# Optimization experiments

Hardware: AMD Instinct MI355X
Metric: run time of the kernel (lower is better)

The kernel has to match this reference:

```python
import jax, jax.numpy as jnp
import numpy as np

LAMBDA_DECAY = 0.01   # self.lambda_decay
ALPHA = 0.95          # self.alpha_continuity
TAU = 0.0             # self.tau
LN_EPS = 1e-5

M, D = 8192, 4096


def layer_norm(x):
    m = jnp.mean(x, axis=-1, keepdims=True)
    v = jnp.var(x, axis=-1, keepdims=True)
    return (x - m) / jnp.sqrt(v + LN_EPS)


def setup_inputs() -> dict:
    key = jax.random.key(0)
    k1, k2, k3, k4, k5 = jax.random.split(key, 5)
    return {
        "states": jax.random.normal(k1, (M, D), dtype=jnp.float32),       # memory bank cell states
        "weights": jax.random.uniform(k2, (M,), dtype=jnp.float32),        # per-cell weights
        "timestamps": jax.random.uniform(k3, (M,), dtype=jnp.float32),     # per-cell timestamps
        "current_state": jax.random.normal(k4, (D,), dtype=jnp.float32),
        "sensed_state": jax.random.normal(k5, (D,), dtype=jnp.float32),    # appended to bank; not in output math
        "t_new": jnp.ones((1,), dtype=jnp.float32),
    }


def reference(states, weights, timestamps, current_state, sensed_state, t_new):
    # Batched per-cell decay update (replaces the Python loop with .item() syncs):
    # cell.weight *= exp(-lambda * |(t_new - cell.timestamp) - tau|)
    decay = jnp.exp(-LAMBDA_DECAY * jnp.abs((t_new[0] - timestamps) - TAU))  # [M]
    w = weights * decay                                                       # [M]

    # scaled_dot single-query attention over the memory bank, modulated by cell weights
    scale = 1.0 / jnp.sqrt(jnp.asarray(states.shape[-1], dtype=states.dtype))
    scores = (states @ current_state) * scale        # [M]
    attn = jax.nn.softmax(scores)                    # [M]
    wa = attn * w
    wa = wa / (jnp.sum(wa) + 1e-9)                   # renormalize by decayed cell weights
    attention_out = wa @ states                      # [D]

    # recursive update: new = alpha * current + (1 - alpha) * attention_out
    new_state = ALPHA * current_state + (1.0 - ALPHA) * attention_out

    # layer norm of the new persistent state
    return layer_norm(new_state)
```

## Files before the change

kernel.cpp:

```cpp
#include <hip/hip_runtime.h>
#include <math.h>

#define LAMBDA_DECAY 0.01f
#define ALPHA 0.95f
#define LN_EPS 1e-5f

#define NB 512
#define RPB 16
#define WPB 8
#define K2Y 32

typedef float v4f __attribute__((ext_vector_type(4)));

static __device__ __forceinline__ float wave_sum_all(float v) {
#pragma unroll
    for (int o = 32; o > 0; o >>= 1) v += __shfl_xor(v, o);
    return v;
}

static __device__ float block_sum(float v, float* sh, int nwaves) {
    int lane = threadIdx.x & 63;
    int w = threadIdx.x >> 6;
    v = wave_sum_all(v);
    if (lane == 0) sh[w] = v;
    __syncthreads();
    float r = 0.0f;
    for (int i = 0; i < nwaves; ++i) r += sh[i];
    __syncthreads();
    return r;
}

__global__ __launch_bounds__(512) void fused_kernel(
    const float* __restrict__ states, const float* __restrict__ cur,
    const float* __restrict__ weights, const float* __restrict__ ts,
    const float* __restrict__ t_new,
    float* __restrict__ partial, float* __restrict__ partE, float* __restrict__ partS,
    int M, int D, float scale)
{
    __shared__ float shp[2][WPB];

    const int wid = threadIdx.x >> 6;
    const int lane = threadIdx.x & 63;
    const int r0 = blockIdx.x * RPB;
    const int f4base = wid * 128 + lane;
    const int rstride = D >> 2;

    const float tn = t_new[0];

    const v4f* c4 = (const v4f*)cur;
    const v4f curp0 = c4[f4base];
    const v4f curp1 = c4[f4base + 64];

    v4f acc0 = (v4f)(0.0f), acc1 = (v4f)(0.0f);
    float E = 0.0f, S = 0.0f;

    const v4f* sp = (const v4f*)states;

    v4f rv[2][2];
    rv[0][0] = sp[(size_t)r0 * rstride + f4base];
    rv[0][1] = sp[(size_t)r0 * rstride + f4base + 64];

#pragma unroll
    for (int r = 0; r < RPB; ++r) {
        const int row = r0 + r;
        const int cb = r & 1;
        const int nb = cb ^ 1;

        if (r + 1 < RPB) {
            rv[nb][0] = sp[(size_t)(row + 1) * rstride + f4base];
            rv[nb][1] = sp[(size_t)(row + 1) * rstride + f4base + 64];
        }

        const v4f a0 = rv[cb][0], a1 = rv[cb][1];

        float d0 = 0.0f, d1 = 0.0f;
        d0 = fmaf(a0[0], curp0[0], d0); d1 = fmaf(a1[0], curp1[0], d1);
        d0 = fmaf(a0[1], curp0[1], d0); d1 = fmaf(a1[1], curp1[1], d1);
        d0 = fmaf(a0[2], curp0[2], d0); d1 = fmaf(a1[2], curp1[2], d1);
        d0 = fmaf(a0[3], curp0[3], d0); d1 = fmaf(a1[3], curp1[3], d1);
        float pd = wave_sum_all(d0 + d1);

        if (lane == 0) shp[cb][wid] = pd;
        __syncthreads();

        float s = 0.0f;
#pragma unroll
        for (int w = 0; w < WPB; ++w) s += shp[cb][w];
        s *= scale;

        const float e = expf(s);
        const float wgt = weights[row] * expf(-LAMBDA_DECAY * fabsf(tn - ts[row]));
        const float p = e * wgt;
        E += e; S += p;

        acc0 += p * a0;
        acc1 += p * a1;
    }

    v4f* pb = (v4f*)(partial + (size_t)blockIdx.x * D);
    pb[f4base] = acc0;
    pb[f4base + 64] = acc1;
    if (threadIdx.x == 0) {
        partE[blockIdx.x] = E;
        partS[blockIdx.x] = S;
    }
}

__global__ __launch_bounds__(256) void reduce_kernel(
    const float* __restrict__ partial, float* __restrict__ attn_raw, int D)
{
    const int col = blockIdx.x * 256 + threadIdx.x;
    const int b0 = blockIdx.y * (NB / K2Y);
    float a0 = 0.0f, a1 = 0.0f, a2 = 0.0f, a3 = 0.0f;
#pragma unroll
    for (int b = 0; b < NB / K2Y; b += 4) {
        a0 += partial[(size_t)(b0 + b) * D + col];
        a1 += partial[(size_t)(b0 + b + 1) * D + col];
        a2 += partial[(size_t)(b0 + b + 2) * D + col];
        a3 += partial[(size_t)(b0 + b + 3) * D + col];
    }
    atomicAdd(&attn_raw[col], (a0 + a1) + (a2 + a3));
}

__global__ __launch_bounds__(1024) void finalize_kernel(
    const float* __restrict__ attn_raw, const float* __restrict__ partE,
    const float* __restrict__ partS, const float* __restrict__ cur,
    float* __restrict__ out, int D)
{
    __shared__ float sh[16];
    const int tid = threadIdx.x;

    float E = 0.0f, S = 0.0f;
    for (int i = tid; i < NB; i += 1024) { E += partE[i]; S += partS[i]; }
    E = block_sum(E, sh, 16);
    S = block_sum(S, sh, 16);
    const float inv = 1.0f / (S + 1e-9f * E);

    float v[4];
    float s = 0.0f, s2 = 0.0f;
#pragma unroll
    for (int k = 0; k < 4; ++k) {
        const int c = tid + k * 1024;
        const float nv = ALPHA * cur[c] + (1.0f - ALPHA) * (attn_raw[c] * inv);
        v[k] = nv;
        s += nv; s2 += nv * nv;
    }
    s = block_sum(s, sh, 16);
    s2 = block_sum(s2, sh, 16);
    const float mean = s / (float)D;
    const float var = s2 / (float)D - mean * mean;
    const float rstd = 1.0f / sqrtf(var + LN_EPS);
#pragma unroll
    for (int k = 0; k < 4; ++k)
        out[tid + k * 1024] = (v[k] - mean) * rstd;
}

extern "C" void kernel_launch(void* const* d_in, const int* in_sizes, int n_in,
                              void* d_out, int out_size, void* d_ws, size_t ws_size,
                              hipStream_t stream) {
    const float* states     = (const float*)d_in[0];
    const float* weights    = (const float*)d_in[1];
    const float* timestamps = (const float*)d_in[2];
    const float* current    = (const float*)d_in[3];
    const float* t_new      = (const float*)d_in[5];
    float* out = (float*)d_out;

    const int M = in_sizes[1];
    const int D = in_sizes[3];

    float* ws       = (float*)d_ws;
    float* partial  = ws;
    float* partE    = partial + (size_t)NB * D;
    float* partS    = partE + NB;
    float* attn_raw = partS + NB;

    const float scale = 1.0f / sqrtf((float)D);

    hipMemsetAsync(attn_raw, 0, (size_t)D * sizeof(float), stream);

    fused_kernel<<<NB, 512, 0, stream>>>(
        states, current, weights, timestamps, t_new,
        partial, partE, partS, M, D, scale);

    {
        dim3 grid(D / 256, K2Y);
        reduce_kernel<<<grid, 256, 0, stream>>>(partial, attn_raw, D);
    }

    finalize_kernel<<<1, 1024, 0, stream>>>(attn_raw, partE, partS, current, out, D);
}
```

Baseline: 39.61 us.

## Fuse reduce and finalize into one tail kernel with last-block counter

Removes the memset by having block 0 of the main kernel zero the accumulator and counter, and merges the column-reduce and layernorm-finalize kernels into one tail kernel. The tail kernel uses a global atomic counter so the last finishing block performs the normalization and layer norm. This cuts two launches and their gaps, but the reduction now runs on only 32 blocks, each summing 256 partial rows per column, which lowers parallelism for reading the 8 MB partial buffer.

Measured after the change: 44.62 us. +12.7%, slower.

```diff
diff --git a/kernel.cpp b/kernel.cpp
--- a/kernel.cpp
+++ b/kernel.cpp
@@ -8,7 +8,7 @@
 #define NB 512
 #define RPB 16
 #define WPB 8
-#define K2Y 32
+#define TB 32
 
 typedef float v4f __attribute__((ext_vector_type(4)));
 
@@ -35,6 +35,7 @@
     const float* __restrict__ weights, const float* __restrict__ ts,
     const float* __restrict__ t_new,
     float* __restrict__ partial, float* __restrict__ partE, float* __restrict__ partS,
+    float* __restrict__ attn_raw, unsigned* __restrict__ counter,
     int M, int D, float scale)
 {
     __shared__ float shp[2][WPB];
@@ -44,6 +45,11 @@
     const int r0 = blockIdx.x * RPB;
     const int f4base = wid * 128 + lane;
     const int rstride = D >> 2;
+
+    if (blockIdx.x == 0) {
+        for (int d = threadIdx.x; d < D; d += 512) attn_raw[d] = 0.0f;
+        if (threadIdx.x == 0) *counter = 0u;
+    }
 
     const float tn = t_new[0];
 
@@ -106,53 +112,67 @@
     }
 }
 
-__global__ __launch_bounds__(256) void reduce_kernel(
-    const float* __restrict__ partial, float* __restrict__ attn_raw, int D)
-{
-    const int col = blockIdx.x * 256 + threadIdx.x;
-    const int b0 = blockIdx.y * (NB / K2Y);
-    float a0 = 0.0f, a1 = 0.0f, a2 = 0.0f, a3 = 0.0f;
-#pragma unroll
-    for (int b = 0; b < NB / K2Y; b += 4) {
-        a0 += partial[(size_t)(b0 + b) * D + col];
-        a1 += partial[(size_t)(b0 + b + 1) * D + col];
-        a2 += partial[(size_t)(b0 + b + 2) * D + col];
-        a3 += partial[(size_t)(b0 + b + 3) * D + col];
-    }
-    atomicAdd(&attn_raw[col], (a0 + a1) + (a2 + a3));
-}
-
-__global__ __launch_bounds__(1024) void finalize_kernel(
-    const float* __restrict__ attn_raw, const float* __restrict__ partE,
+__global__ __launch_bounds__(256) void tail_kernel(
+    const float* __restrict__ partial, const float* __restrict__ partE,
     const float* __restrict__ partS, const float* __restrict__ cur,
+    float* __restrict__ attn_raw, unsigned* __restrict__ counter,
     float* __restrict__ out, int D)
 {
-    __shared__ float sh[16];
-    const int tid = threadIdx.x;
+    __shared__ float shc[128];
+    __shared__ float sh16[16];
+    __shared__ unsigned sdone;
+
+    const int cid = threadIdx.x & 127;
+    const int half = threadIdx.x >> 7;
+    const int col = blockIdx.x * 128 + cid;
+
+    {
+        const int b0 = half * (NB / 2);
+        float a0 = 0.0f, a1 = 0.0f, a2 = 0.0f, a3 = 0.0f;
+        for (int b = 0; b < NB / 2; b += 4) {
+            a0 += partial[(size_t)(b0 + b) * D + col];
+            a1 += partial[(size_t)(b0 + b + 1) * D + col];
+            a2 += partial[(size_t)(b0 + b + 2) * D + col];
+            a3 += partial[(size_t)(b0 + b + 3) * D + col];
+        }
+        const float a = (a0 + a1) + (a2 + a3);
+        if (half) shc[cid] = a;
+        __syncthreads();
+        if (!half) atomicAdd(&attn_raw[col], a + shc[cid]);
+    }
+
+    __threadfence();
+    __syncthreads();
+    if (threadIdx.x == 0) sdone = atomicAdd(counter, 1u);
+    __syncthreads();
+    if (sdone != TB - 1) return;
+
+    if (threadIdx.x == 0) *counter = 0u;
+    __threadfence();
 
     float E = 0.0f, S = 0.0f;
-    for (int i = tid; i < NB; i += 1024) { E += partE[i]; S += partS[i]; }
-    E = block_sum(E, sh, 16);
-    S = block_sum(S, sh, 16);
+    for (int i = threadIdx.x; i < NB; i += 256) { E += partE[i]; S += partS[i]; }
+    E = block_sum(E, sh16, 4);
+    S = block_sum(S, sh16, 4);
     const float inv = 1.0f / (S + 1e-9f * E);
 
-    float v[4];
+    float v[16];
     float s = 0.0f, s2 = 0.0f;
 #pragma unroll
-    for (int k = 0; k < 4; ++k) {
-        const int c = tid + k * 1024;
+    for (int k = 0; k < 16; ++k) {
+        const int c = threadIdx.x + k * 256;
         const float nv = ALPHA * cur[c] + (1.0f - ALPHA) * (attn_raw[c] * inv);
         v[k] = nv;
         s += nv; s2 += nv * nv;
     }
-    s = block_sum(s, sh, 16);
-    s2 = block_sum(s2, sh, 16);
+    s = block_sum(s, sh16, 4);
+    s2 = block_sum(s2, sh16, 4);
     const float mean = s / (float)D;
     const float var = s2 / (float)D - mean * mean;
     const float rstd = 1.0f / sqrtf(var + LN_EPS);
 #pragma unroll
-    for (int k = 0; k < 4; ++k)
-        out[tid + k * 1024] = (v[k] - mean) * rstd;
+    for (int k = 0; k < 16; ++k)
+        out[threadIdx.x + k * 256] = (v[k] - mean) * rstd;
 }
 
 extern "C" void kernel_launch(void* const* d_in, const int* in_sizes, int n_in,
@@ -168,24 +188,19 @@
     const int M = in_sizes[1];
     const int D = in_sizes[3];
 
-    float* ws       = (float*)d_ws;
-    float* partial  = ws;
-    float* partE    = partial + (size_t)NB * D;
-    float* partS    = partE + NB;
-    float* attn_raw = partS + NB;
+    float* ws        = (float*)d_ws;
+    float* partial   = ws;
+    float* partE     = partial + (size_t)NB * D;
+    float* partS     = partE + NB;
+    float* attn_raw  = partS + NB;
+    unsigned* counter = (unsigned*)(attn_raw + D);
 
     const float scale = 1.0f / sqrtf((float)D);
-
-    hipMemsetAsync(attn_raw, 0, (size_t)D * sizeof(float), stream);
 
     fused_kernel<<<NB, 512, 0, stream>>>(
         states, current, weights, timestamps, t_new,
-        partial, partE, partS, M, D, scale);
-
-    {
-        dim3 grid(D / 256, K2Y);
-        reduce_kernel<<<grid, 256, 0, stream>>>(partial, attn_raw, D);
-    }
-
-    finalize_kernel<<<1, 1024, 0, stream>>>(attn_raw, partE, partS, current, out, D);
-}
+        partial, partE, partS, attn_raw, counter, M, D, scale);
+
+    tail_kernel<<<TB, 256, 0, stream>>>(
+        partial, partE, partS, current, attn_raw, counter, out, D);
+}
```
